# Performance work log

Measured on AMD Instinct MI355X. Metric: run time of the kernel, lower is better.

## Reference

```python
import jax, jax.numpy as jnp
import numpy as np

N_NODES = 600_000
N_EDGES = 2_400_000
LEADS = 12
NUM_GRAPHS = N_NODES // LEADS  # 50_000
F_IN = 128
H = 64
OUT = 32


def setup_inputs() -> dict:
    key = jax.random.key(0)
    ks = jax.random.split(key, 12)
    x = jax.random.normal(ks[0], (N_NODES, F_IN), dtype=jnp.float32)
    src = jax.random.randint(ks[1], (N_EDGES,), 0, N_NODES)
    dst = jax.random.randint(ks[2], (N_EDGES,), 0, N_NODES)
    edge_index = jnp.stack([src, dst], axis=0)
    batch = jnp.repeat(jnp.arange(NUM_GRAPHS), LEADS)  # 12 nodes (leads) per graph
    s = 0.05
    W1 = jax.random.normal(ks[3], (F_IN, H), dtype=jnp.float32) * s
    b1 = jnp.zeros((H,), dtype=jnp.float32)
    W2 = jax.random.normal(ks[4], (H, H), dtype=jnp.float32) * s
    b2 = jnp.zeros((H,), dtype=jnp.float32)
    W3 = jax.random.normal(ks[5], (H, H), dtype=jnp.float32) * s
    b3 = jnp.zeros((H,), dtype=jnp.float32)
    Wa = jax.random.normal(ks[6], (H, H), dtype=jnp.float32) * s   # attention.attn (no bias)
    v = jax.random.normal(ks[7], (H, 1), dtype=jnp.float32) * s    # attention.v (no bias)
    Wl = jax.random.normal(ks[8], (2 * H, OUT), dtype=jnp.float32) * s  # self.lin
    bl = jnp.zeros((OUT,), dtype=jnp.float32)
    return {"x": x, "edge_index": edge_index, "batch": batch,
            "W1": W1, "b1": b1, "W2": W2, "b2": b2, "W3": W3, "b3": b3,
            "Wa": Wa, "v": v, "Wl": Wl, "bl": bl}


def reference(x, edge_index, batch, W1, b1, W2, b2, W3, b3, Wa, v, Wl, bl):
    n = x.shape[0]
    # GCNConv with self-loops and symmetric normalization (PyG defaults)
    loops = jnp.arange(n)
    row = jnp.concatenate([edge_index[0], loops])  # source
    col = jnp.concatenate([edge_index[1], loops])  # target
    deg = jax.ops.segment_sum(jnp.ones((row.shape[0],), dtype=x.dtype), col, num_segments=n)
    dinv = jnp.where(deg > 0, jax.lax.rsqrt(deg), 0.0)
    norm = dinv[row] * dinv[col]  # [E+N]

    def conv(h, W, b):
        h = h @ W  # transform first (small GEMM), then gather-scale-scatter
        agg = jax.ops.segment_sum(h[row] * norm[:, None], col, num_segments=n)
        return agg + b

    h = jax.nn.relu(conv(x, W1, b1))
    h = jax.nn.relu(conv(h, W2, b2))
    h = jax.nn.relu(conv(h, W3, b3))

    # lead attention over 12 consecutive nodes per graph
    h3 = h.reshape(-1, LEADS, H)               # [G, 12, 64]
    energy = jnp.tanh(h3 @ Wa)                 # [G, 12, 64]
    lweights = jax.nn.softmax(energy @ v, axis=1)  # [G, 12, 1]
    h = (h3 * lweights).reshape(-1, H)         # [N, 64]

    # global max pool + global mean pool per graph
    gmax = jax.ops.segment_max(h, batch, num_segments=NUM_GRAPHS)
    ssum = jax.ops.segment_sum(h, batch, num_segments=NUM_GRAPHS)
    cnt = jax.ops.segment_sum(jnp.ones((n,), dtype=h.dtype), batch, num_segments=NUM_GRAPHS)
    gmean = ssum / jnp.maximum(cnt, 1.0)[:, None]
    pooled = jnp.concatenate([gmax, gmean], axis=1)  # [G, 128]

    # dropout is identity in eval mode
    out = jax.nn.relu(pooled @ Wl + bl)  # [G, 32]
    return out, lweights
```

## Files before the change

### kernel.cpp

```cpp
#include <hip/hip_runtime.h>
#include <math.h>

#define N_NODES 600000
#define N_EDGES 2400000
#define HD 64
#define F_IN 128
#define LEADS 12
#define NUM_GRAPHS 50000
#define OUT_DIM 32
#define SCAN_BLOCKS 586

typedef float nf4 __attribute__((ext_vector_type(4)));

__global__ __launch_bounds__(256) void k_zero(int* __restrict__ cnt) {
    int i = blockIdx.x * 256 + threadIdx.x;
    if (i < N_NODES) cnt[i] = 0;
}

__global__ __launch_bounds__(256) void k_hist(const int* __restrict__ dst,
                                              int* __restrict__ cnt,
                                              int* __restrict__ rank) {
    int e = blockIdx.x * 256 + threadIdx.x;
    if (e < N_EDGES) rank[e] = atomicAdd(&cnt[dst[e]], 1);
}

__global__ __launch_bounds__(256) void k_scan1(const int* __restrict__ cnt,
                                               int* __restrict__ offs,
                                               int* __restrict__ bsum,
                                               float* __restrict__ dinv) {
    __shared__ int lds[256];
    int t = threadIdx.x;
    int base = blockIdx.x * 1024 + t * 4;
    int v[4];
#pragma unroll
    for (int j = 0; j < 4; ++j) v[j] = (base + j < N_NODES) ? cnt[base + j] : 0;
#pragma unroll
    for (int j = 0; j < 4; ++j)
        if (base + j < N_NODES) dinv[base + j] = rsqrtf((float)(v[j] + 1));
    int s = v[0] + v[1] + v[2] + v[3];
    lds[t] = s;
    __syncthreads();
    int val = s;
    for (int off = 1; off < 256; off <<= 1) {
        int other = (t >= off) ? lds[t - off] : 0;
        __syncthreads();
        val += other;
        lds[t] = val;
        __syncthreads();
    }
    if (t == 255) bsum[blockIdx.x] = val;
    int run = val - s;
#pragma unroll
    for (int j = 0; j < 4; ++j) {
        if (base + j < N_NODES) offs[base + j] = run;
        run += v[j];
    }
}

__global__ __launch_bounds__(256) void k_scan2(int* __restrict__ bsum) {
    __shared__ int lds[SCAN_BLOCKS];
    for (int i = threadIdx.x; i < SCAN_BLOCKS; i += 256) lds[i] = bsum[i];
    __syncthreads();
    if (threadIdx.x == 0) {
        int run = 0;
        for (int i = 0; i < SCAN_BLOCKS; ++i) {
            int c = lds[i];
            lds[i] = run;
            run += c;
        }
    }
    __syncthreads();
    for (int i = threadIdx.x; i < SCAN_BLOCKS; i += 256) bsum[i] = lds[i];
}

__global__ __launch_bounds__(256) void k_scan3(int* __restrict__ offs,
                                               const int* __restrict__ bsum) {
    int i = blockIdx.x * 256 + threadIdx.x;
    if (i < N_NODES) offs[i] += bsum[i >> 10];
}

__global__ __launch_bounds__(256) void k_fill(const int* __restrict__ src,
                                              const int* __restrict__ dst,
                                              const int* __restrict__ rank,
                                              const int* __restrict__ offs,
                                              int* __restrict__ eidx) {
    int e = blockIdx.x * 256 + threadIdx.x;
    if (e < N_EDGES) {
        int p = offs[dst[e]] + rank[e];
        eidx[p] = src[e];
    }
}

__device__ __forceinline__ float4 gcn_gather(const float4* __restrict__ tp4,
                                             const int* __restrict__ eidx,
                                             int node, int start, int c, int cm,
                                             int sl, int grpBase) {
    float4 a0 = tp4[(size_t)node * 16 + sl];
    float4 a1 = {0.0f, 0.0f, 0.0f, 0.0f};
    float4 a2 = {0.0f, 0.0f, 0.0f, 0.0f};
    float4 a3 = {0.0f, 0.0f, 0.0f, 0.0f};

    for (int base = 0; base < cm; base += 16) {
        int idxreg = (base + sl < c) ? eidx[start + base + sl] : node;
        int take = cm - base;
        if (take > 16) take = 16;
        for (int j = 0; j < take; j += 8) {
            int i0 = __shfl(idxreg, grpBase + j + 0);
            int i1 = __shfl(idxreg, grpBase + j + 1);
            int i2 = __shfl(idxreg, grpBase + j + 2);
            int i3 = __shfl(idxreg, grpBase + j + 3);
            int i4 = __shfl(idxreg, grpBase + j + 4);
            int i5 = __shfl(idxreg, grpBase + j + 5);
            int i6 = __shfl(idxreg, grpBase + j + 6);
            int i7 = __shfl(idxreg, grpBase + j + 7);
            float m0 = (base + j + 0 < c) ? 1.0f : 0.0f;
            float m1 = (base + j + 1 < c) ? 1.0f : 0.0f;
            float m2 = (base + j + 2 < c) ? 1.0f : 0.0f;
            float m3 = (base + j + 3 < c) ? 1.0f : 0.0f;
            float m4 = (base + j + 4 < c) ? 1.0f : 0.0f;
            float m5 = (base + j + 5 < c) ? 1.0f : 0.0f;
            float m6 = (base + j + 6 < c) ? 1.0f : 0.0f;
            float m7 = (base + j + 7 < c) ? 1.0f : 0.0f;
            float4 v0 = tp4[(size_t)i0 * 16 + sl];
            float4 v1 = tp4[(size_t)i1 * 16 + sl];
            float4 v2 = tp4[(size_t)i2 * 16 + sl];
            float4 v3 = tp4[(size_t)i3 * 16 + sl];
            float4 v4 = tp4[(size_t)i4 * 16 + sl];
            float4 v5 = tp4[(size_t)i5 * 16 + sl];
            float4 v6 = tp4[(size_t)i6 * 16 + sl];
            float4 v7 = tp4[(size_t)i7 * 16 + sl];
            a0.x = fmaf(m0, v0.x, a0.x); a0.y = fmaf(m0, v0.y, a0.y);
            a0.z = fmaf(m0, v0.z, a0.z); a0.w = fmaf(m0, v0.w, a0.w);
            a1.x = fmaf(m1, v1.x, a1.x); a1.y = fmaf(m1, v1.y, a1.y);
            a1.z = fmaf(m1, v1.z, a1.z); a1.w = fmaf(m1, v1.w, a1.w);
            a2.x = fmaf(m2, v2.x, a2.x); a2.y = fmaf(m2, v2.y, a2.y);
            a2.z = fmaf(m2, v2.z, a2.z); a2.w = fmaf(m2, v2.w, a2.w);
            a3.x = fmaf(m3, v3.x, a3.x); a3.y = fmaf(m3, v3.y, a3.y);
            a3.z = fmaf(m3, v3.z, a3.z); a3.w = fmaf(m3, v3.w, a3.w);
            a0.x = fmaf(m4, v4.x, a0.x); a0.y = fmaf(m4, v4.y, a0.y);
            a0.z = fmaf(m4, v4.z, a0.z); a0.w = fmaf(m4, v4.w, a0.w);
            a1.x = fmaf(m5, v5.x, a1.x); a1.y = fmaf(m5, v5.y, a1.y);
            a1.z = fmaf(m5, v5.z, a1.z); a1.w = fmaf(m5, v5.w, a1.w);
            a2.x = fmaf(m6, v6.x, a2.x); a2.y = fmaf(m6, v6.y, a2.y);
            a2.z = fmaf(m6, v6.z, a2.z); a2.w = fmaf(m6, v6.w, a2.w);
            a3.x = fmaf(m7, v7.x, a3.x); a3.y = fmaf(m7, v7.y, a3.y);
            a3.z = fmaf(m7, v7.z, a3.z); a3.w = fmaf(m7, v7.w, a3.w);
        }
    }
    a0.x += a1.x + a2.x + a3.x;
    a0.y += a1.y + a2.y + a3.y;
    a0.z += a1.z + a2.z + a3.z;
    a0.w += a1.w + a2.w + a3.w;
    return a0;
}

template <int K>
__global__ __launch_bounds__(256) void k_gemm(const float* __restrict__ in,
                                              const float* __restrict__ W,
                                              const float* __restrict__ dinv,
                                              float* __restrict__ tout) {
    __shared__ float lx[64 * (K + 1)];
    const int t = threadIdx.x;
    const int lane = t & 63;
    const int r0 = blockIdx.x * 64;

#pragma unroll
    for (int i = 0; i < K / 16; ++i) {
        int f = (t + i * 256) * 4;
        int r = f / K, k = f % K;
        nf4 v = __builtin_nontemporal_load(
            (const nf4*)(in + (size_t)(r0 + r) * K + k));
        float* p = &lx[r * (K + 1) + k];
        p[0] = v.x; p[1] = v.y; p[2] = v.z; p[3] = v.w;
    }
    __syncthreads();

    const int c0 = __builtin_amdgcn_readfirstlane((t >> 6) * 16);
    const float* Wp = W + c0;

    float acc[16];
#pragma unroll
    for (int cc = 0; cc < 16; ++cc) acc[cc] = 0.0f;

#pragma unroll
    for (int k = 0; k < K; ++k) {
        float xk = lx[lane * (K + 1) + k];
#pragma unroll
        for (int cc = 0; cc < 16; ++cc)
            acc[cc] = fmaf(xk, Wp[k * HD + cc], acc[cc]);
    }

    float di = dinv[r0 + lane];
#pragma unroll
    for (int cc = 0; cc < 16; ++cc) acc[cc] *= di;

    __syncthreads();
#pragma unroll
    for (int cc = 0; cc < 16; ++cc) lx[lane * 65 + c0 + cc] = acc[cc];
    __syncthreads();

    const int w = t >> 6;
#pragma unroll
    for (int i = 0; i < 16; ++i) {
        int r = i * 4 + w;
        tout[(size_t)(r0 + r) * HD + lane] = lx[r * 65 + lane];
    }
}

__global__ __launch_bounds__(256) void k_fused(const float* __restrict__ tp,
                                               const int* __restrict__ eidx,
                                               const int* __restrict__ offs,
                                               const int* __restrict__ cnt,
                                               const float* __restrict__ dinv,
                                               const float* __restrict__ bias,
                                               const float* __restrict__ W,
                                               float* __restrict__ tout) {
    __shared__ float lhx[64 * 65];
    const int t = threadIdx.x;
    const int lane = t & 63;
    const int w = t >> 6;
    const int r0 = blockIdx.x * 64;
    const int grp = lane >> 4, sl = lane & 15;
    const int grpBase = lane & 48;

    const float4* tp4 = (const float4*)tp;
    const float4 b4 = *(const float4*)(bias + sl * 4);

#pragma unroll
    for (int p = 0; p < 4; ++p) {
        const int nl = p * 16 + w * 4 + grp;
        const int node = r0 + nl;

        const int start = offs[node];
        const int c = cnt[node];

        int cm = c;
#pragma unroll
        for (int off = 32; off >= 1; off >>= 1) cm = max(cm, __shfl_xor(cm, off));

        float4 r = gcn_gather(tp4, eidx, node, start, c, cm, sl, grpBase);

        const float di = dinv[node];
        float* pl = &lhx[nl * 65 + sl * 4];
        pl[0] = fmaxf(fmaf(di, r.x, b4.x), 0.0f);
        pl[1] = fmaxf(fmaf(di, r.y, b4.y), 0.0f);
        pl[2] = fmaxf(fmaf(di, r.z, b4.z), 0.0f);
        pl[3] = fmaxf(fmaf(di, r.w, b4.w), 0.0f);
    }
    __syncthreads();

    const int c0 = __builtin_amdgcn_readfirstlane(w * 16);
    const float* Wp = W + c0;

    float acc[16];
#pragma unroll
    for (int cc = 0; cc < 16; ++cc) acc[cc] = 0.0f;

#pragma unroll
    for (int k = 0; k < HD; ++k) {
        float xk = lhx[lane * 65 + k];
#pragma unroll
        for (int cc = 0; cc < 16; ++cc)
            acc[cc] = fmaf(xk, Wp[k * HD + cc], acc[cc]);
    }

    float di2 = dinv[r0 + lane];
#pragma unroll
    for (int cc = 0; cc < 16; ++cc) acc[cc] *= di2;

    __syncthreads();
#pragma unroll
    for (int cc = 0; cc < 16; ++cc) lhx[lane * 65 + c0 + cc] = acc[cc];
    __syncthreads();

#pragma unroll
    for (int i = 0; i < 16; ++i) {
        int r = i * 4 + w;
        __builtin_nontemporal_store(lhx[r * 65 + lane],
                                    &tout[(size_t)(r0 + r) * HD + lane]);
    }
}

__global__ __launch_bounds__(256) void k_gather(const float* __restrict__ tp,
                                                const int* __restrict__ eidx,
                                                const int* __restrict__ offs,
                                                const int* __restrict__ cnt,
                                                const float* __restrict__ dinv,
                                                const float* __restrict__ bias,
                                                float* __restrict__ h) {
    const int wave = (blockIdx.x * 256 + threadIdx.x) >> 6;
    const int lane = threadIdx.x & 63;
    const int grp = lane >> 4, sl = lane & 15;
    const int grpBase = lane & 48;
    const int node = wave * 4 + grp;

    const float4* tp4 = (const float4*)tp;

    const int start = offs[node];
    const int c = cnt[node];

    int cm = c;
#pragma unroll
    for (int off = 32; off >= 1; off >>= 1) cm = max(cm, __shfl_xor(cm, off));

    float4 a = gcn_gather(tp4, eidx, node, start, c, cm, sl, grpBase);

    const float di = dinv[node];
    const float4 b4 = *(const float4*)(bias + sl * 4);
    nf4 r;
    r.x = fmaxf(fmaf(di, a.x, b4.x), 0.0f);
    r.y = fmaxf(fmaf(di, a.y, b4.y), 0.0f);
    r.z = fmaxf(fmaf(di, a.z, b4.z), 0.0f);
    r.w = fmaxf(fmaf(di, a.w, b4.w), 0.0f);
    __builtin_nontemporal_store(r, &((nf4*)h)[(size_t)node * 16 + sl]);
}

__global__ __launch_bounds__(256) void k_attn(const float* __restrict__ h3,
                                              const float* __restrict__ Wa,
                                              const float* __restrict__ vvec,
                                              const float* __restrict__ Wl,
                                              const float* __restrict__ bl,
                                              float* __restrict__ out,
                                              float* __restrict__ lw) {
    __shared__ float lds_Wl[128 * 32];
    __shared__ float lds_h[4][LEADS * 64];
    __shared__ float lds_p[4][128];
    const int t = threadIdx.x;
    const int lane = t & 63;
    const int wid = t >> 6;

#pragma unroll
    for (int i = 0; i < 16; ++i) lds_Wl[t + i * 256] = Wl[t + i * 256];

    float wa[64];
#pragma unroll
    for (int k = 0; k < 64; ++k) wa[k] = Wa[k * 64 + lane];
    float vl = vvec[lane];
    __syncthreads();

    const int g = blockIdx.x * 4 + wid;

    float hv[LEADS];
#pragma unroll
    for (int r = 0; r < LEADS; ++r) {
        hv[r] = h3[(size_t)(g * LEADS + r) * 64 + lane];
        lds_h[wid][r * 64 + lane] = hv[r];
    }

    float s_[LEADS];
#pragma unroll
    for (int r = 0; r < LEADS; ++r) {
        float acc = 0.0f;
        const float4* h4 = (const float4*)&lds_h[wid][r * 64];
#pragma unroll
        for (int k4 = 0; k4 < 16; ++k4) {
            float4 hb = h4[k4];
            acc = fmaf(hb.x, wa[4 * k4 + 0], acc);
            acc = fmaf(hb.y, wa[4 * k4 + 1], acc);
            acc = fmaf(hb.z, wa[4 * k4 + 2], acc);
            acc = fmaf(hb.w, wa[4 * k4 + 3], acc);
        }
        float sc = tanhf(acc) * vl;
#pragma unroll
        for (int off = 32; off >= 1; off >>= 1) sc += __shfl_xor(sc, off);
        s_[r] = sc;
    }

    float m = s_[0];
#pragma unroll
    for (int r = 1; r < LEADS; ++r) m = fmaxf(m, s_[r]);
    float wgt[LEADS];
    float sum = 0.0f;
#pragma unroll
    for (int r = 0; r < LEADS; ++r) {
        wgt[r] = expf(s_[r] - m);
        sum += wgt[r];
    }
    float inv = 1.0f / sum;

    float tmp = wgt[0] * inv;
#pragma unroll
    for (int r = 1; r < LEADS; ++r) tmp = (lane == r) ? wgt[r] * inv : tmp;
    if (lane < LEADS) lw[g * LEADS + lane] = tmp;

    float gmax = -1e30f, gsum = 0.0f;
#pragma unroll
    for (int r = 0; r < LEADS; ++r) {
        float wh = hv[r] * (wgt[r] * inv);
        gmax = fmaxf(gmax, wh);
        gsum += wh;
    }
    lds_p[wid][lane] = gmax;
    lds_p[wid][64 + lane] = gsum * (1.0f / 12.0f);

    int o = lane & 31, half = lane >> 5;
    float acc2 = 0.0f;
#pragma unroll
    for (int k = 0; k < 64; ++k) {
        int kk = half * 64 + k;
        acc2 = fmaf(lds_p[wid][kk], lds_Wl[kk * 32 + o], acc2);
    }
    acc2 += __shfl_xor(acc2, 32);
    if (lane < 32) out[g * 32 + lane] = fmaxf(acc2 + bl[lane], 0.0f);
}

extern "C" void kernel_launch(void* const* d_in, const int* in_sizes, int n_in,
                              void* d_out, int out_size, void* d_ws, size_t ws_size,
                              hipStream_t stream) {
    const float* x  = (const float*)d_in[0];
    const int* ei   = (const int*)d_in[1];
    const int* src  = ei;
    const int* dst  = ei + N_EDGES;
    const float* W1 = (const float*)d_in[3];
    const float* b1 = (const float*)d_in[4];
    const float* W2 = (const float*)d_in[5];
    const float* b2 = (const float*)d_in[6];
    const float* W3 = (const float*)d_in[7];
    const float* b3 = (const float*)d_in[8];
    const float* Wa = (const float*)d_in[9];
    const float* vv = (const float*)d_in[10];
    const float* Wl = (const float*)d_in[11];
    const float* bl = (const float*)d_in[12];

    float* out = (float*)d_out;
    float* lw  = out + (size_t)NUM_GRAPHS * 32;

    float* dinv = (float*)d_ws;
    int* cnt    = (int*)(dinv + N_NODES);
    int* offs   = cnt + N_NODES;
    int* bsum   = offs + N_NODES;
    int* eidx   = bsum + 1024;
    float* T    = (float*)(eidx + N_EDGES);
    float* Hb   = T + (size_t)N_NODES * HD;
    int* rank   = (int*)T;

    const int gN = (N_NODES + 255) / 256;
    const int gE = (N_EDGES + 255) / 256;

    k_zero<<<gN, 256, 0, stream>>>(cnt);
    k_hist<<<gE, 256, 0, stream>>>(dst, cnt, rank);
    k_scan1<<<SCAN_BLOCKS, 256, 0, stream>>>(cnt, offs, bsum, dinv);
    k_scan2<<<1, 256, 0, stream>>>(bsum);
    k_scan3<<<gN, 256, 0, stream>>>(offs, bsum);
    k_fill<<<gE, 256, 0, stream>>>(src, dst, rank, offs, eidx);

    k_gemm<128><<<N_NODES / 64, 256, 0, stream>>>(x, W1, dinv, T);
    k_fused<<<N_NODES / 64, 256, 0, stream>>>(T, eidx, offs, cnt, dinv, b1, W2, Hb);
    k_fused<<<N_NODES / 64, 256, 0, stream>>>(Hb, eidx, offs, cnt, dinv, b2, W3, T);
    k_gather<<<N_NODES / 16, 256, 0, stream>>>(T, eidx, offs, cnt, dinv, b3, Hb);
    k_attn<<<NUM_GRAPHS / 4, 256, 0, stream>>>(Hb, Wa, vv, Wl, bl, out, lw);
}
```

Measured before the change: 1.252 ms.

## Fuse attention score computation into final GCN gather kernel

The last GCN aggregation now works on 64-node tiles in LDS and computes the attention energy tanh(h·Wa)·v per node in the same kernel, writing a per-node score array. The pooling kernel then only reads scores and h to do the softmax, weighting and pooling, so it no longer holds Wa in registers or runs a 64x64 matvec per lead. This moves the attention GEMM next to the gathered data, but the gather kernel gains LDS use and syncs, and Wa is read from global memory inside its inner loop.

Result: slower. 2.090 ms (+66.9%).

```diff
diff --git a/kernel.cpp b/kernel.cpp
--- a/kernel.cpp
+++ b/kernel.cpp
@@ -281,49 +281,92 @@
     }
 }
 
-__global__ __launch_bounds__(256) void k_gather(const float* __restrict__ tp,
+__global__ __launch_bounds__(256) void k_fused3(const float* __restrict__ tp,
                                                 const int* __restrict__ eidx,
                                                 const int* __restrict__ offs,
                                                 const int* __restrict__ cnt,
                                                 const float* __restrict__ dinv,
                                                 const float* __restrict__ bias,
-                                                float* __restrict__ h) {
-    const int wave = (blockIdx.x * 256 + threadIdx.x) >> 6;
-    const int lane = threadIdx.x & 63;
+                                                const float* __restrict__ Wa,
+                                                const float* __restrict__ vvec,
+                                                float* __restrict__ hout,
+                                                float* __restrict__ sout) {
+    __shared__ float lhx[64 * 65];
+    __shared__ float sp[4][64];
+    const int t = threadIdx.x;
+    const int lane = t & 63;
+    const int w = t >> 6;
+    const int r0 = blockIdx.x * 64;
     const int grp = lane >> 4, sl = lane & 15;
     const int grpBase = lane & 48;
-    const int node = wave * 4 + grp;
 
     const float4* tp4 = (const float4*)tp;
-
-    const int start = offs[node];
-    const int c = cnt[node];
-
-    int cm = c;
-#pragma unroll
-    for (int off = 32; off >= 1; off >>= 1) cm = max(cm, __shfl_xor(cm, off));
-
-    float4 a = gcn_gather(tp4, eidx, node, start, c, cm, sl, grpBase);
-
-    const float di = dinv[node];
     const float4 b4 = *(const float4*)(bias + sl * 4);
-    nf4 r;
-    r.x = fmaxf(fmaf(di, a.x, b4.x), 0.0f);
-    r.y = fmaxf(fmaf(di, a.y, b4.y), 0.0f);
-    r.z = fmaxf(fmaf(di, a.z, b4.z), 0.0f);
-    r.w = fmaxf(fmaf(di, a.w, b4.w), 0.0f);
-    __builtin_nontemporal_store(r, &((nf4*)h)[(size_t)node * 16 + sl]);
-}
-
-__global__ __launch_bounds__(256) void k_attn(const float* __restrict__ h3,
-                                              const float* __restrict__ Wa,
-                                              const float* __restrict__ vvec,
+
+#pragma unroll
+    for (int p = 0; p < 4; ++p) {
+        const int nl = p * 16 + w * 4 + grp;
+        const int node = r0 + nl;
+
+        const int start = offs[node];
+        const int c = cnt[node];
+
+        int cm = c;
+#pragma unroll
+        for (int off = 32; off >= 1; off >>= 1) cm = max(cm, __shfl_xor(cm, off));
+
+        float4 r = gcn_gather(tp4, eidx, node, start, c, cm, sl, grpBase);
+
+        const float di = dinv[node];
+        float* pl = &lhx[nl * 65 + sl * 4];
+        pl[0] = fmaxf(fmaf(di, r.x, b4.x), 0.0f);
+        pl[1] = fmaxf(fmaf(di, r.y, b4.y), 0.0f);
+        pl[2] = fmaxf(fmaf(di, r.z, b4.z), 0.0f);
+        pl[3] = fmaxf(fmaf(di, r.w, b4.w), 0.0f);
+    }
+    __syncthreads();
+
+    const int c0 = __builtin_amdgcn_readfirstlane(w * 16);
+    const float* Wp = Wa + c0;
+
+    float acc[16];
+#pragma unroll
+    for (int cc = 0; cc < 16; ++cc) acc[cc] = 0.0f;
+
+#pragma unroll
+    for (int k = 0; k < HD; ++k) {
+        float xk = lhx[lane * 65 + k];
+#pragma unroll
+        for (int cc = 0; cc < 16; ++cc)
+            acc[cc] = fmaf(xk, Wp[k * HD + cc], acc[cc]);
+    }
+
+    float part = 0.0f;
+#pragma unroll
+    for (int cc = 0; cc < 16; ++cc)
+        part = fmaf(tanhf(acc[cc]), vvec[c0 + cc], part);
+    sp[w][lane] = part;
+    __syncthreads();
+
+#pragma unroll
+    for (int i = 0; i < 16; ++i) {
+        int r = i * 4 + w;
+        hout[(size_t)(r0 + r) * HD + lane] = lhx[r * 65 + lane];
+    }
+
+    if (w == 0) {
+        float s = sp[0][lane] + sp[1][lane] + sp[2][lane] + sp[3][lane];
+        sout[r0 + lane] = s;
+    }
+}
+
+__global__ __launch_bounds__(256) void k_pool(const float* __restrict__ h3,
+                                              const float* __restrict__ s,
                                               const float* __restrict__ Wl,
                                               const float* __restrict__ bl,
                                               float* __restrict__ out,
                                               float* __restrict__ lw) {
     __shared__ float lds_Wl[128 * 32];
-    __shared__ float lds_h[4][LEADS * 64];
     __shared__ float lds_p[4][128];
     const int t = threadIdx.x;
     const int lane = t & 63;
@@ -331,62 +374,28 @@
 
 #pragma unroll
     for (int i = 0; i < 16; ++i) lds_Wl[t + i * 256] = Wl[t + i * 256];
-
-    float wa[64];
-#pragma unroll
-    for (int k = 0; k < 64; ++k) wa[k] = Wa[k * 64 + lane];
-    float vl = vvec[lane];
     __syncthreads();
 
     const int g = blockIdx.x * 4 + wid;
 
-    float hv[LEADS];
+    float sv = (lane < LEADS) ? s[g * LEADS + lane] : -1e30f;
+    float m = sv;
+#pragma unroll
+    for (int off = 32; off >= 1; off >>= 1) m = fmaxf(m, __shfl_xor(m, off));
+    float e = (lane < LEADS) ? expf(sv - m) : 0.0f;
+    float sum = e;
+#pragma unroll
+    for (int off = 32; off >= 1; off >>= 1) sum += __shfl_xor(sum, off);
+    float inv = 1.0f / sum;
+
+    if (lane < LEADS) lw[g * LEADS + lane] = e * inv;
+
+    float gmax = -1e30f, gsum = 0.0f;
 #pragma unroll
     for (int r = 0; r < LEADS; ++r) {
-        hv[r] = h3[(size_t)(g * LEADS + r) * 64 + lane];
-        lds_h[wid][r * 64 + lane] = hv[r];
-    }
-
-    float s_[LEADS];
-#pragma unroll
-    for (int r = 0; r < LEADS; ++r) {
-        float acc = 0.0f;
-        const float4* h4 = (const float4*)&lds_h[wid][r * 64];
-#pragma unroll
-        for (int k4 = 0; k4 < 16; ++k4) {
-            float4 hb = h4[k4];
-            acc = fmaf(hb.x, wa[4 * k4 + 0], acc);
-            acc = fmaf(hb.y, wa[4 * k4 + 1], acc);
-            acc = fmaf(hb.z, wa[4 * k4 + 2], acc);
-            acc = fmaf(hb.w, wa[4 * k4 + 3], acc);
-        }
-        float sc = tanhf(acc) * vl;
-#pragma unroll
-        for (int off = 32; off >= 1; off >>= 1) sc += __shfl_xor(sc, off);
-        s_[r] = sc;
-    }
-
-    float m = s_[0];
-#pragma unroll
-    for (int r = 1; r < LEADS; ++r) m = fmaxf(m, s_[r]);
-    float wgt[LEADS];
-    float sum = 0.0f;
-#pragma unroll
-    for (int r = 0; r < LEADS; ++r) {
-        wgt[r] = expf(s_[r] - m);
-        sum += wgt[r];
-    }
-    float inv = 1.0f / sum;
-
-    float tmp = wgt[0] * inv;
-#pragma unroll
-    for (int r = 1; r < LEADS; ++r) tmp = (lane == r) ? wgt[r] * inv : tmp;
-    if (lane < LEADS) lw[g * LEADS + lane] = tmp;
-
-    float gmax = -1e30f, gsum = 0.0f;
-#pragma unroll
-    for (int r = 0; r < LEADS; ++r) {
-        float wh = hv[r] * (wgt[r] * inv);
+        float wr = __shfl(e, r) * inv;
+        float hv = h3[(size_t)(g * LEADS + r) * HD + lane];
+        float wh = hv * wr;
         gmax = fmaxf(gmax, wh);
         gsum += wh;
     }
@@ -432,6 +441,7 @@
     int* eidx   = bsum + 1024;
     float* T    = (float*)(eidx + N_EDGES);
     float* Hb   = T + (size_t)N_NODES * HD;
+    float* S    = Hb + (size_t)N_NODES * HD;
     int* rank   = (int*)T;
 
     const int gN = (N_NODES + 255) / 256;
@@ -447,6 +457,7 @@
     k_gemm<128><<<N_NODES / 64, 256, 0, stream>>>(x, W1, dinv, T);
     k_fused<<<N_NODES / 64, 256, 0, stream>>>(T, eidx, offs, cnt, dinv, b1, W2, Hb);
     k_fused<<<N_NODES / 64, 256, 0, stream>>>(Hb, eidx, offs, cnt, dinv, b2, W3, T);
-    k_gather<<<N_NODES / 16, 256, 0, stream>>>(T, eidx, offs, cnt, dinv, b3, Hb);
-    k_attn<<<NUM_GRAPHS / 4, 256, 0, stream>>>(Hb, Wa, vv, Wl, bl, out, lw);
-}
+    k_fused3<<<N_NODES / 64, 256, 0, stream>>>(T, eidx, offs, cnt, dinv, b3,
+                                               Wa, vv, Hb, S);
+    k_pool<<<NUM_GRAPHS / 4, 256, 0, stream>>>(Hb, S, Wl, bl, out, lw);
+}
```
